# Optimization experiments

Measured on AMD Instinct MI355X. Metric: run time of the kernel, lower is better.

The kernel has to match this reference:

```python
import jax, jax.numpy as jnp
import numpy as np

PI = float(np.pi)

def erp_xyz_coords(h, w):
    # matches calculate_erp_coord: pixel grid -> uv -> unit-sphere xyz
    yy, xx = jnp.meshgrid(jnp.linspace(0.0, h - 1.0, h), jnp.linspace(0.0, w - 1.0, w), indexing='ij')
    u = (xx - (w / 2.0 + 0.5)) / w * 2.0 * PI
    v = (yy - (h / 2.0 + 0.5)) / h * PI
    xyz = jnp.stack([jnp.cos(v) * jnp.sin(u), jnp.sin(v), jnp.cos(v) * jnp.cos(u)], axis=-1)
    return xyz.reshape(h * w, 3)  # (HW, 3)


def setup_inputs() -> dict:
    key = jax.random.key(0)
    ks = jax.random.split(key, 16)
    B, C, H, W = 1, 128, 16, 32
    Nkv = 1280
    s = 0.02
    inp = {
        'erp_feature': jax.random.normal(ks[0], (B, C, H, W), jnp.float32),
        'ico_feature': jax.random.normal(ks[1], (B, Nkv, C), jnp.float32),
        'ico_coord': jax.random.normal(ks[2], (B, Nkv, 3), jnp.float32),
        # SA branch params (torch Linear: y = x @ W.T + b, W is (out,in))
        'Wq_sa': jax.random.normal(ks[3], (C, C), jnp.float32) * s,
        'Wkv_sa': jax.random.normal(ks[4], (2 * C, C), jnp.float32) * s,
        'proj_sa_w': jax.random.normal(ks[5], (C, C), jnp.float32) * s,
        'proj_sa_b': jnp.zeros((C,), jnp.float32),
        # DA branch params
        'Wq_da': jax.random.normal(ks[6], (C, C), jnp.float32) * s,
        'Wkv_da': jax.random.normal(ks[7], (2 * C, C), jnp.float32) * s,
        'Wdelta': jax.random.normal(ks[8], (C, 3), jnp.float32) * s,
        'proj_da_w': jax.random.normal(ks[9], (C, C), jnp.float32) * s,
        'proj_da_b': jnp.zeros((C,), jnp.float32),
        # gates
        'gate_sa_w': jax.random.normal(ks[10], (C, 2 * C), jnp.float32) * s,
        'gate_da_w': jax.random.normal(ks[11], (C, 2 * C), jnp.float32) * s,
    }
    return inp


def _forward(erp_feature, ico_feature, ico_coord,
             Wq_sa, Wkv_sa, proj_sa_w, proj_sa_b,
             Wq_da, Wkv_da, Wdelta, proj_da_w, proj_da_b,
             gate_sa_w, gate_da_w):
    B, C, H, W = erp_feature.shape
    Nq = H * W
    q = erp_feature.reshape(B, C, Nq).transpose(0, 2, 1)  # (B, Nq, C)
    qc = erp_xyz_coords(H, W)[None]                        # (1, Nq, 3) broadcasts over B

    # ---- SA branch (iteration = 1) ----
    q_sa = q @ Wq_sa.T                                     # (B, Nq, C)
    kv_sa = (ico_feature @ Wkv_sa.T).reshape(B, -1, 2, C)
    k_sa, v_sa = kv_sa[:, :, 0], kv_sa[:, :, 1]
    attn_sa = jax.nn.softmax(jnp.einsum('bqc,bkc->bqk', q_sa, k_sa) * (C ** -0.5), axis=-1)
    out_sa = jnp.einsum('bqk,bkc->bqc', attn_sa, v_sa)
    # faithful to torch: .transpose(1,2).reshape(B, Nq, C) scrambles layout
    out_sa = out_sa.transpose(0, 2, 1).reshape(B, Nq, C)
    sa = out_sa @ proj_sa_w.T + proj_sa_b

    # ---- DA branch (iteration = 1) ----
    q_da = q @ Wq_da.T
    kv_da = (ico_feature @ Wkv_da.T).reshape(B, -1, 2, C)
    k_da, v_da = kv_da[:, :, 0], kv_da[:, :, 1]
    # feature affinity: sum_c exp(-|q_c - k_c|)   -> (B, Nq, Nkv)
    feat_aff = jnp.exp(-jnp.abs(q_da[:, :, None, :] - k_da[:, None, :, :])).sum(-1)
    # positional term: (exp(-|dq - dk|) @ Wdelta.T).sum(-1) == exp(...) . Wdelta.sum(0)
    pos_exp = jnp.exp(-jnp.abs(qc[:, :, None, :] - ico_coord[:, None, :, :]))  # (B,Nq,Nkv,3)
    pos_aff = jnp.einsum('bqkt,t->bqk', pos_exp, Wdelta.sum(0))
    attn_da = jax.nn.softmax((feat_aff + pos_aff) * (1.0 / C), axis=-1)
    out_da = jnp.einsum('bqk,bkc->bqc', attn_da, v_da)
    da = out_da @ proj_da_w.T + proj_da_b

    # ---- gated fusion ----
    cat = jnp.concatenate([sa, da], axis=-1)               # (B, Nq, 2C)
    sa_factor = jax.nn.sigmoid(cat @ gate_sa_w.T)
    da_factor = jax.nn.sigmoid(cat @ gate_da_w.T)
    fused = sa_factor * sa + da_factor * da                # (B, Nq, C)
    return fused.reshape(B, H, W, C).transpose(0, 3, 1, 2)  # (B, C, H, W)


def reference(erp_feature, ico_feature, ico_coord,
              Wq_sa, Wkv_sa, proj_sa_w, proj_sa_b,
              Wq_da, Wkv_da, Wdelta, proj_da_w, proj_da_b,
              gate_sa_w, gate_da_w):
    return _forward(erp_feature, ico_feature, ico_coord,
                    Wq_sa, Wkv_sa, proj_sa_w, proj_sa_b,
                    Wq_da, Wkv_da, Wdelta, proj_da_w, proj_da_b,
                    gate_sa_w, gate_da_w)
```

## Files before the change

kernel.cpp:

```cpp
#include <hip/hip_runtime.h>
#include <math.h>

#define NQ   512
#define NKV  1280
#define CDIM 128

#define OFF_WDSUM 0
#define OFF_SUMS  16
#define OFF_QSA   1056
#define OFF_QDA   66592
#define OFF_KSAT  132128
#define OFF_VSA   295968
#define OFF_KDAT  459808
#define OFF_VDA   623648
#define OFF_OUT   787488

__global__ __launch_bounds__(256) void prep_kernel(
    const float* __restrict__ erp, const float* __restrict__ ico,
    const float* __restrict__ wq_sa, const float* __restrict__ wq_da,
    const float* __restrict__ wkv_sa, const float* __restrict__ wkv_da,
    const float* __restrict__ wdelta, float* __restrict__ ws)
{
  int bx = blockIdx.x, t = threadIdx.x;
  if (bx < 320) {
    __shared__ float x4[4 * CDIM];
    int k0 = bx * 4;
    for (int i = t; i < 512; i += 256) {
      int ky = i >> 7, j = i & 127;
      x4[j * 4 + ky] = ico[(k0 + ky) * CDIM + j];
    }
    __syncthreads();
    const float4* wsa4 = (const float4*)(wkv_sa + t * CDIM);
    const float4* wda4 = (const float4*)(wkv_da + t * CDIM);
    float as0=0,as1=0,as2=0,as3=0, ad0=0,ad1=0,ad2=0,ad3=0;
    #pragma unroll 4
    for (int j4 = 0; j4 < 32; ++j4) {
      float4 wsv = wsa4[j4];
      float4 wdv = wda4[j4];
      float4 x0 = *(const float4*)&x4[(j4 * 4 + 0) * 4];
      float4 x1 = *(const float4*)&x4[(j4 * 4 + 1) * 4];
      float4 x2 = *(const float4*)&x4[(j4 * 4 + 2) * 4];
      float4 x3 = *(const float4*)&x4[(j4 * 4 + 3) * 4];
      as0 = fmaf(wsv.x, x0.x, as0); as1 = fmaf(wsv.x, x0.y, as1);
      as2 = fmaf(wsv.x, x0.z, as2); as3 = fmaf(wsv.x, x0.w, as3);
      ad0 = fmaf(wdv.x, x0.x, ad0); ad1 = fmaf(wdv.x, x0.y, ad1);
      ad2 = fmaf(wdv.x, x0.z, ad2); ad3 = fmaf(wdv.x, x0.w, ad3);
      as0 = fmaf(wsv.y, x1.x, as0); as1 = fmaf(wsv.y, x1.y, as1);
      as2 = fmaf(wsv.y, x1.z, as2); as3 = fmaf(wsv.y, x1.w, as3);
      ad0 = fmaf(wdv.y, x1.x, ad0); ad1 = fmaf(wdv.y, x1.y, ad1);
      ad2 = fmaf(wdv.y, x1.z, ad2); ad3 = fmaf(wdv.y, x1.w, ad3);
      as0 = fmaf(wsv.z, x2.x, as0); as1 = fmaf(wsv.z, x2.y, as1);
      as2 = fmaf(wsv.z, x2.z, as2); as3 = fmaf(wsv.z, x2.w, as3);
      ad0 = fmaf(wdv.z, x2.x, ad0); ad1 = fmaf(wdv.z, x2.y, ad1);
      ad2 = fmaf(wdv.z, x2.z, ad2); ad3 = fmaf(wdv.z, x2.w, ad3);
      as0 = fmaf(wsv.w, x3.x, as0); as1 = fmaf(wsv.w, x3.y, as1);
      as2 = fmaf(wsv.w, x3.z, as2); as3 = fmaf(wsv.w, x3.w, as3);
      ad0 = fmaf(wdv.w, x3.x, ad0); ad1 = fmaf(wdv.w, x3.y, ad1);
      ad2 = fmaf(wdv.w, x3.z, ad2); ad3 = fmaf(wdv.w, x3.w, ad3);
    }
    if (t < 128) {
      *(float4*)(ws + OFF_KSAT + t * NKV + k0) = make_float4(as0, as1, as2, as3);
      *(float4*)(ws + OFF_KDAT + t * NKV + k0) = make_float4(ad0, ad1, ad2, ad3);
    } else {
      int c = t - 128;
      ws[OFF_VSA + (k0 + 0) * CDIM + c] = as0;
      ws[OFF_VSA + (k0 + 1) * CDIM + c] = as1;
      ws[OFF_VSA + (k0 + 2) * CDIM + c] = as2;
      ws[OFF_VSA + (k0 + 3) * CDIM + c] = as3;
      ws[OFF_VDA + (k0 + 0) * CDIM + c] = ad0;
      ws[OFF_VDA + (k0 + 1) * CDIM + c] = ad1;
      ws[OFF_VDA + (k0 + 2) * CDIM + c] = ad2;
      ws[OFF_VDA + (k0 + 3) * CDIM + c] = ad3;
    }
  } else if (bx < 448) {
    __shared__ float q4[4 * CDIM];
    int n0 = (bx - 320) * 4;
    for (int i = t; i < 512; i += 256)
      q4[i] = erp[(i >> 2) * NQ + n0 + (i & 3)];
    __syncthreads();
    const float* w = (t < 128) ? wq_sa : wq_da;
    int c = t & 127;
    const float4* w4 = (const float4*)(w + c * CDIM);
    float a0 = 0.f, a1 = 0.f, a2 = 0.f, a3 = 0.f;
    #pragma unroll 8
    for (int j4 = 0; j4 < 32; ++j4) {
      float4 wv = w4[j4];
      float4 q0 = *(const float4*)&q4[(j4 * 4 + 0) * 4];
      float4 q1 = *(const float4*)&q4[(j4 * 4 + 1) * 4];
      float4 q2 = *(const float4*)&q4[(j4 * 4 + 2) * 4];
      float4 q3 = *(const float4*)&q4[(j4 * 4 + 3) * 4];
      a0 = fmaf(wv.x, q0.x, a0); a1 = fmaf(wv.x, q0.y, a1);
      a2 = fmaf(wv.x, q0.z, a2); a3 = fmaf(wv.x, q0.w, a3);
      a0 = fmaf(wv.y, q1.x, a0); a1 = fmaf(wv.y, q1.y, a1);
      a2 = fmaf(wv.y, q1.z, a2); a3 = fmaf(wv.y, q1.w, a3);
      a0 = fmaf(wv.z, q2.x, a0); a1 = fmaf(wv.z, q2.y, a1);
      a2 = fmaf(wv.z, q2.z, a2); a3 = fmaf(wv.z, q2.w, a3);
      a0 = fmaf(wv.w, q3.x, a0); a1 = fmaf(wv.w, q3.y, a1);
      a2 = fmaf(wv.w, q3.z, a2); a3 = fmaf(wv.w, q3.w, a3);
    }
    float* o = ws + ((t < 128) ? OFF_QSA : OFF_QDA);
    o[(n0 + 0) * CDIM + c] = a0;
    o[(n0 + 1) * CDIM + c] = a1;
    o[(n0 + 2) * CDIM + c] = a2;
    o[(n0 + 3) * CDIM + c] = a3;
  } else if (bx == 448) {
    *(float4*)(ws + OFF_SUMS + t * 4) = make_float4(0.f, 0.f, 0.f, 0.f);
    if (t < 3) {
      float s = 0.f;
      for (int i = 0; i < 128; ++i) s += wdelta[i * 3 + t];
      ws[OFF_WDSUM + t] = s;
    }
  } else {
    int base = OFF_OUT + (bx - 449) * 1024 + t * 4;
    *(float4*)(ws + base) = make_float4(0.f, 0.f, 0.f, 0.f);
  }
}

__global__ __launch_bounds__(256) void attn_kernel(
    const float* __restrict__ coord, float* __restrict__ ws)
{
  __shared__ __align__(16) float qjf[4 * CDIM];
  __shared__ __align__(16) float psc[2][4][128];
  __shared__ __align__(16) float posk[4][128];
  __shared__ __align__(16) float se[4][128];
  __shared__ float red[2][4];
  __shared__ float qcr[4][3];
  __shared__ float wdl[3];
  int b = blockIdx.x, t = threadIdx.x;
  int br = (b < 1280) ? 1 : 0;
  int bb = br ? b : b - 1280;
  int g = bb / 10, z = bb - g * 10;
  int n0 = g * 4, k0 = z * 128;

  const float* qsrc = ws + (br ? OFF_QDA : OFF_QSA);
  for (int i = t; i < 512; i += 256) {
    int r = i & 3, j = i >> 2;
    qjf[j * 4 + r] = qsrc[(n0 + r) * CDIM + j];
  }
  if (br) {
    if (t < 4) {
      int n = n0 + t;
      float x = (float)(n & 31), y = (float)(n >> 5);
      float u  = (x - 16.5f) * 0.19634954084936207f;
      float vv = (y -  8.5f) * 0.19634954084936207f;
      float cv = cosf(vv);
      qcr[t][0] = cv * sinf(u);
      qcr[t][1] = sinf(vv);
      qcr[t][2] = cv * cosf(u);
    }
    if (t >= 64 && t < 67) wdl[t - 64] = ws[OFF_WDSUM + t - 64];
  }
  __syncthreads();

  int kl = t & 127, jh = t >> 7;
  int k = k0 + kl;
  {
    const float* kp = ws + (br ? OFF_KDAT : OFF_KSAT) + k + jh * 64 * NKV;
    const float4* qj = (const float4*)&qjf[jh * 64 * 4];
    float a0 = 0.f, a1 = 0.f, a2 = 0.f, a3 = 0.f;
    if (br) {
      #pragma unroll 4
      for (int j = 0; j < 64; ++j) {
        float kv = kp[j * NKV];
        float4 q = qj[j];
        a0 += __expf(-fabsf(q.x - kv)); a1 += __expf(-fabsf(q.y - kv));
        a2 += __expf(-fabsf(q.z - kv)); a3 += __expf(-fabsf(q.w - kv));
      }
    } else {
      #pragma unroll 8
      for (int j = 0; j < 64; ++j) {
        float kv = kp[j * NKV];
        float4 q = qj[j];
        a0 = fmaf(q.x, kv, a0); a1 = fmaf(q.y, kv, a1);
        a2 = fmaf(q.z, kv, a2); a3 = fmaf(q.w, kv, a3);
      }
    }
    psc[jh][0][kl] = a0; psc[jh][1][kl] = a1;
    psc[jh][2][kl] = a2; psc[jh][3][kl] = a3;
    if (br && jh == 1) {
      float c0 = coord[k * 3], c1 = coord[k * 3 + 1], c2 = coord[k * 3 + 2];
      float w0 = wdl[0], w1 = wdl[1], w2 = wdl[2];
      #pragma unroll
      for (int r = 0; r < 4; ++r)
        posk[r][kl] = w0 * __expf(-fabsf(qcr[r][0] - c0))
                    + w1 * __expf(-fabsf(qcr[r][1] - c1))
                    + w2 * __expf(-fabsf(qcr[r][2] - c2));
    }
  }
  __syncthreads();

  if (t < 128) {
    const float scl = 0.088388347648318447f;
    const float i128 = 0.0078125f;
    float s[4];
    #pragma unroll
    for (int r = 0; r < 4; ++r) {
      float tot = psc[0][r][t] + psc[1][r][t];
      float l = br ? (tot + posk[r][t]) * i128 : tot * scl;
      float e = __expf(l);
      se[r][t] = e;
      s[r] = e;
    }
    #pragma unroll
    for (int o = 32; o > 0; o >>= 1) {
      s[0] += __shfl_down(s[0], o, 64); s[1] += __shfl_down(s[1], o, 64);
      s[2] += __shfl_down(s[2], o, 64); s[3] += __shfl_down(s[3], o, 64);
    }
    if ((t & 63) == 0) {
      int w = t >> 6;
      red[w][0] = s[0]; red[w][1] = s[1]; red[w][2] = s[2]; red[w][3] = s[3];
    }
  }
  __syncthreads();
  if (t < 4)
    atomicAdd(ws + OFF_SUMS + br * 512 + n0 + t, red[0][t] + red[1][t]);

  int c = t & 127, h = t >> 7;
  const float* vp = ws + (br ? OFF_VDA : OFF_VSA) + k0 * CDIM + c;
  float acc0 = 0.f, acc1 = 0.f;
  #pragma unroll 4
  for (int ko = 0; ko < 128; ko += 4) {
    float4 pa = *(const float4*)&se[h][ko];
    float4 pb = *(const float4*)&se[h + 2][ko];
    float v0 = vp[(ko + 0) * CDIM];
    float v1 = vp[(ko + 1) * CDIM];
    float v2 = vp[(ko + 2) * CDIM];
    float v3 = vp[(ko + 3) * CDIM];
    acc0 = fmaf(pa.x, v0, acc0); acc1 = fmaf(pb.x, v0, acc1);
    acc0 = fmaf(pa.y, v1, acc0); acc1 = fmaf(pb.y, v1, acc1);
    acc0 = fmaf(pa.z, v2, acc0); acc1 = fmaf(pb.z, v2, acc1);
    acc0 = fmaf(pa.w, v3, acc0); acc1 = fmaf(pb.w, v3, acc1);
  }
  float* op = ws + OFF_OUT + br * (NQ * CDIM);
  atomicAdd(op + (n0 + h) * CDIM + c,     acc0);
  atomicAdd(op + (n0 + h + 2) * CDIM + c, acc1);
}

__global__ __launch_bounds__(256) void finalize_kernel(
    const float* __restrict__ psa, const float* __restrict__ bsa,
    const float* __restrict__ pda, const float* __restrict__ bda,
    const float* __restrict__ gsa, const float* __restrict__ gda,
    float* __restrict__ out, float* __restrict__ ws)
{
  __shared__ float sain[2][CDIM];
  __shared__ float dain[2][CDIM];
  __shared__ float cat[2][2 * CDIM];
  __shared__ float gl[2][2][CDIM];
  int i0 = blockIdx.x * 2, t = threadIdx.x;
  int h = t >> 7, c = t & 127;
  #pragma unroll
  for (int rr = 0; rr < 2; ++rr) {
    int i = i0 + rr;
    if (h == 0) {
      int row = (i & 3) * 128 + c;
      float s = ws[OFF_SUMS + row];
      sain[rr][c] = ws[OFF_OUT + row * CDIM + (i >> 2)] / s;
    } else {
      float s = ws[OFF_SUMS + 512 + i];
      dain[rr][c] = ws[OFF_OUT + NQ * CDIM + i * CDIM + c] / s;
    }
  }
  __syncthreads();
  {
    const float4* w4 = (const float4*)((h ? pda : psa) + c * CDIM);
    const float* in0 = h ? dain[0] : sain[0];
    const float* in1 = h ? dain[1] : sain[1];
    float a0 = 0, a1 = 0, b0 = 0, b1 = 0;
    #pragma unroll 8
    for (int j4 = 0; j4 < 32; ++j4) {
      float4 wv = w4[j4];
      float4 x0 = *(const float4*)&in0[j4 * 4];
      float4 x1 = *(const float4*)&in1[j4 * 4];
      a0 = fmaf(wv.x, x0.x, a0); a1 = fmaf(wv.y, x0.y, a1);
      a0 = fmaf(wv.z, x0.z, a0); a1 = fmaf(wv.w, x0.w, a1);
      b0 = fmaf(wv.x, x1.x, b0); b1 = fmaf(wv.y, x1.y, b1);
      b0 = fmaf(wv.z, x1.z, b0); b1 = fmaf(wv.w, x1.w, b1);
    }
    float bias = h ? bda[c] : bsa[c];
    cat[0][h * CDIM + c] = bias + a0 + a1;
    cat[1][h * CDIM + c] = bias + b0 + b1;
  }
  __syncthreads();
  {
    const float4* g4 = (const float4*)((h ? gda : gsa) + c * 2 * CDIM);
    float a0 = 0, a1 = 0, b0 = 0, b1 = 0;
    #pragma unroll 8
    for (int j4 = 0; j4 < 64; ++j4) {
      float4 gv = g4[j4];
      float4 c0 = *(const float4*)&cat[0][j4 * 4];
      float4 c1 = *(const float4*)&cat[1][j4 * 4];
      a0 = fmaf(gv.x, c0.x, a0); a1 = fmaf(gv.y, c0.y, a1);
      a0 = fmaf(gv.z, c0.z, a0); a1 = fmaf(gv.w, c0.w, a1);
      b0 = fmaf(gv.x, c1.x, b0); b1 = fmaf(gv.y, c1.y, b1);
      b0 = fmaf(gv.z, c1.z, b0); b1 = fmaf(gv.w, c1.w, b1);
    }
    gl[0][h][c] = 1.0f / (1.0f + __expf(-(a0 + a1)));
    gl[1][h][c] = 1.0f / (1.0f + __expf(-(b0 + b1)));
  }
  __syncthreads();
  {
    int i = i0 + h;
    out[c * NQ + i] = gl[h][0][c] * cat[h][c] + gl[h][1][c] * cat[h][CDIM + c];
  }
}

extern "C" void kernel_launch(void* const* d_in, const int* in_sizes, int n_in,
                              void* d_out, int out_size, void* d_ws, size_t ws_size,
                              hipStream_t stream)
{
  (void)in_sizes; (void)n_in; (void)out_size; (void)ws_size;
  const float* erp       = (const float*)d_in[0];
  const float* ico       = (const float*)d_in[1];
  const float* coord     = (const float*)d_in[2];
  const float* wq_sa     = (const float*)d_in[3];
  const float* wkv_sa    = (const float*)d_in[4];
  const float* proj_sa_w = (const float*)d_in[5];
  const float* proj_sa_b = (const float*)d_in[6];
  const float* wq_da     = (const float*)d_in[7];
  const float* wkv_da    = (const float*)d_in[8];
  const float* wdelta    = (const float*)d_in[9];
  const float* proj_da_w = (const float*)d_in[10];
  const float* proj_da_b = (const float*)d_in[11];
  const float* gate_sa   = (const float*)d_in[12];
  const float* gate_da   = (const float*)d_in[13];
  float* out = (float*)d_out;
  float* ws  = (float*)d_ws;

  hipLaunchKernelGGL(prep_kernel, dim3(577), dim3(256), 0, stream,
                     erp, ico, wq_sa, wq_da, wkv_sa, wkv_da, wdelta, ws);
  hipLaunchKernelGGL(attn_kernel, dim3(2560), dim3(256), 0, stream,
                     coord, ws);
  hipLaunchKernelGGL(finalize_kernel, dim3(256), dim3(256), 0, stream,
                     proj_sa_w, proj_sa_b, proj_da_w, proj_da_b,
                     gate_sa, gate_da, out, ws);
}
```

Before: 142.8 us.

## Retile attention to 8 queries x 256 keys per block with exp2 prescaling

Each attention block now handles 8 queries and 256 keys instead of 4 queries and 128 keys, with each thread owning a whole key across all 128 channels. This drops the split-channel partial-score smem stage and quarters the grid size. Each loaded K and V value is reused across twice as many queries, and there are fewer atomics per output. The DA branch and the softmax now use exp2f, with log2(e) folded into the stored Q/K projections and coordinates. The trade-offs are more registers per thread (8 accumulators), fewer blocks to spread across CUs, and interleaved SA/DA block ordering.

Measured after the change: 173.9 us. 21.7% more time.

```diff
diff --git a/kernel.cpp b/kernel.cpp
--- a/kernel.cpp
+++ b/kernel.cpp
@@ -4,6 +4,7 @@
 #define NQ   512
 #define NKV  1280
 #define CDIM 128
+#define L2E  1.4426950408889634f
 
 #define OFF_WDSUM 0
 #define OFF_SUMS  16
@@ -60,7 +61,8 @@
     }
     if (t < 128) {
       *(float4*)(ws + OFF_KSAT + t * NKV + k0) = make_float4(as0, as1, as2, as3);
-      *(float4*)(ws + OFF_KDAT + t * NKV + k0) = make_float4(ad0, ad1, ad2, ad3);
+      *(float4*)(ws + OFF_KDAT + t * NKV + k0) =
+          make_float4(ad0 * L2E, ad1 * L2E, ad2 * L2E, ad3 * L2E);
     } else {
       int c = t - 128;
       ws[OFF_VSA + (k0 + 0) * CDIM + c] = as0;
@@ -98,11 +100,12 @@
       a0 = fmaf(wv.w, q3.x, a0); a1 = fmaf(wv.w, q3.y, a1);
       a2 = fmaf(wv.w, q3.z, a2); a3 = fmaf(wv.w, q3.w, a3);
     }
+    float sc = (t < 128) ? 1.0f : L2E;
     float* o = ws + ((t < 128) ? OFF_QSA : OFF_QDA);
-    o[(n0 + 0) * CDIM + c] = a0;
-    o[(n0 + 1) * CDIM + c] = a1;
-    o[(n0 + 2) * CDIM + c] = a2;
-    o[(n0 + 3) * CDIM + c] = a3;
+    o[(n0 + 0) * CDIM + c] = a0 * sc;
+    o[(n0 + 1) * CDIM + c] = a1 * sc;
+    o[(n0 + 2) * CDIM + c] = a2 * sc;
+    o[(n0 + 3) * CDIM + c] = a3 * sc;
   } else if (bx == 448) {
     *(float4*)(ws + OFF_SUMS + t * 4) = make_float4(0.f, 0.f, 0.f, 0.f);
     if (t < 3) {
@@ -119,121 +122,159 @@
 __global__ __launch_bounds__(256) void attn_kernel(
     const float* __restrict__ coord, float* __restrict__ ws)
 {
-  __shared__ __align__(16) float qjf[4 * CDIM];
-  __shared__ __align__(16) float psc[2][4][128];
-  __shared__ __align__(16) float posk[4][128];
-  __shared__ __align__(16) float se[4][128];
-  __shared__ float red[2][4];
-  __shared__ float qcr[4][3];
+  __shared__ __align__(16) float qjf[128][8];
+  __shared__ __align__(16) float se[8][256];
+  __shared__ float red[4][8];
+  __shared__ float qcr[8][3];
   __shared__ float wdl[3];
   int b = blockIdx.x, t = threadIdx.x;
-  int br = (b < 1280) ? 1 : 0;
-  int bb = br ? b : b - 1280;
-  int g = bb / 10, z = bb - g * 10;
-  int n0 = g * 4, k0 = z * 128;
+  int br = b & 1;
+  int bb = b >> 1;
+  int g = bb / 5, z = bb - g * 5;
+  int n0 = g * 8, k0 = z * 256;
 
   const float* qsrc = ws + (br ? OFF_QDA : OFF_QSA);
-  for (int i = t; i < 512; i += 256) {
-    int r = i & 3, j = i >> 2;
-    qjf[j * 4 + r] = qsrc[(n0 + r) * CDIM + j];
+  {
+    int j = t & 127, r0 = t >> 7;
+    qjf[j][r0]     = qsrc[(n0 + r0)     * CDIM + j];
+    qjf[j][r0 + 2] = qsrc[(n0 + r0 + 2) * CDIM + j];
+    qjf[j][r0 + 4] = qsrc[(n0 + r0 + 4) * CDIM + j];
+    qjf[j][r0 + 6] = qsrc[(n0 + r0 + 6) * CDIM + j];
   }
   if (br) {
-    if (t < 4) {
+    if (t < 8) {
       int n = n0 + t;
       float x = (float)(n & 31), y = (float)(n >> 5);
       float u  = (x - 16.5f) * 0.19634954084936207f;
       float vv = (y -  8.5f) * 0.19634954084936207f;
       float cv = cosf(vv);
-      qcr[t][0] = cv * sinf(u);
-      qcr[t][1] = sinf(vv);
-      qcr[t][2] = cv * cosf(u);
-    }
-    if (t >= 64 && t < 67) wdl[t - 64] = ws[OFF_WDSUM + t - 64];
-  }
-  __syncthreads();
-
-  int kl = t & 127, jh = t >> 7;
-  int k = k0 + kl;
-  {
-    const float* kp = ws + (br ? OFF_KDAT : OFF_KSAT) + k + jh * 64 * NKV;
-    const float4* qj = (const float4*)&qjf[jh * 64 * 4];
-    float a0 = 0.f, a1 = 0.f, a2 = 0.f, a3 = 0.f;
-    if (br) {
-      #pragma unroll 4
-      for (int j = 0; j < 64; ++j) {
-        float kv = kp[j * NKV];
-        float4 q = qj[j];
-        a0 += __expf(-fabsf(q.x - kv)); a1 += __expf(-fabsf(q.y - kv));
-        a2 += __expf(-fabsf(q.z - kv)); a3 += __expf(-fabsf(q.w - kv));
-      }
-    } else {
-      #pragma unroll 8
-      for (int j = 0; j < 64; ++j) {
-        float kv = kp[j * NKV];
-        float4 q = qj[j];
-        a0 = fmaf(q.x, kv, a0); a1 = fmaf(q.y, kv, a1);
-        a2 = fmaf(q.z, kv, a2); a3 = fmaf(q.w, kv, a3);
-      }
-    }
-    psc[jh][0][kl] = a0; psc[jh][1][kl] = a1;
-    psc[jh][2][kl] = a2; psc[jh][3][kl] = a3;
-    if (br && jh == 1) {
-      float c0 = coord[k * 3], c1 = coord[k * 3 + 1], c2 = coord[k * 3 + 2];
-      float w0 = wdl[0], w1 = wdl[1], w2 = wdl[2];
-      #pragma unroll
-      for (int r = 0; r < 4; ++r)
-        posk[r][kl] = w0 * __expf(-fabsf(qcr[r][0] - c0))
-                    + w1 * __expf(-fabsf(qcr[r][1] - c1))
-                    + w2 * __expf(-fabsf(qcr[r][2] - c2));
-    }
-  }
-  __syncthreads();
-
-  if (t < 128) {
-    const float scl = 0.088388347648318447f;
-    const float i128 = 0.0078125f;
-    float s[4];
+      qcr[t][0] = cv * sinf(u) * L2E;
+      qcr[t][1] = sinf(vv) * L2E;
+      qcr[t][2] = cv * cosf(u) * L2E;
+    }
+    if (t >= 64 && t < 67) wdl[t - 64] = ws[OFF_WDSUM + (t - 64)];
+  }
+  __syncthreads();
+
+  int kl = t, k = k0 + kl;
+  float acc[8];
+  #pragma unroll
+  for (int r = 0; r < 8; ++r) acc[r] = 0.f;
+
+  if (br) {
+    const float* kp = ws + OFF_KDAT + k;
+    #pragma unroll 2
+    for (int j = 0; j < 128; ++j) {
+      float kv = kp[j * NKV];
+      float4 qa = *(const float4*)&qjf[j][0];
+      float4 qb = *(const float4*)&qjf[j][4];
+      acc[0] += exp2f(-fabsf(qa.x - kv));
+      acc[1] += exp2f(-fabsf(qa.y - kv));
+      acc[2] += exp2f(-fabsf(qa.z - kv));
+      acc[3] += exp2f(-fabsf(qa.w - kv));
+      acc[4] += exp2f(-fabsf(qb.x - kv));
+      acc[5] += exp2f(-fabsf(qb.y - kv));
+      acc[6] += exp2f(-fabsf(qb.z - kv));
+      acc[7] += exp2f(-fabsf(qb.w - kv));
+    }
+  } else {
+    const float* kp = ws + OFF_KSAT + k;
+    #pragma unroll 4
+    for (int j = 0; j < 128; ++j) {
+      float kv = kp[j * NKV];
+      float4 qa = *(const float4*)&qjf[j][0];
+      float4 qb = *(const float4*)&qjf[j][4];
+      acc[0] = fmaf(qa.x, kv, acc[0]);
+      acc[1] = fmaf(qa.y, kv, acc[1]);
+      acc[2] = fmaf(qa.z, kv, acc[2]);
+      acc[3] = fmaf(qa.w, kv, acc[3]);
+      acc[4] = fmaf(qb.x, kv, acc[4]);
+      acc[5] = fmaf(qb.y, kv, acc[5]);
+      acc[6] = fmaf(qb.z, kv, acc[6]);
+      acc[7] = fmaf(qb.w, kv, acc[7]);
+    }
+  }
+
+  float e[8];
+  if (br) {
+    float c0 = coord[3 * k]     * L2E;
+    float c1 = coord[3 * k + 1] * L2E;
+    float c2 = coord[3 * k + 2] * L2E;
+    float w0 = wdl[0], w1 = wdl[1], w2 = wdl[2];
     #pragma unroll
-    for (int r = 0; r < 4; ++r) {
-      float tot = psc[0][r][t] + psc[1][r][t];
-      float l = br ? (tot + posk[r][t]) * i128 : tot * scl;
-      float e = __expf(l);
-      se[r][t] = e;
-      s[r] = e;
-    }
+    for (int r = 0; r < 8; ++r) {
+      float pos = w0 * exp2f(-fabsf(qcr[r][0] - c0))
+                + w1 * exp2f(-fabsf(qcr[r][1] - c1))
+                + w2 * exp2f(-fabsf(qcr[r][2] - c2));
+      e[r] = exp2f((acc[r] + pos) * (L2E / 128.0f));
+    }
+  } else {
+    const float scl = 0.088388347648318447f * L2E;
     #pragma unroll
-    for (int o = 32; o > 0; o >>= 1) {
-      s[0] += __shfl_down(s[0], o, 64); s[1] += __shfl_down(s[1], o, 64);
-      s[2] += __shfl_down(s[2], o, 64); s[3] += __shfl_down(s[3], o, 64);
-    }
-    if ((t & 63) == 0) {
-      int w = t >> 6;
-      red[w][0] = s[0]; red[w][1] = s[1]; red[w][2] = s[2]; red[w][3] = s[3];
-    }
-  }
-  __syncthreads();
-  if (t < 4)
-    atomicAdd(ws + OFF_SUMS + br * 512 + n0 + t, red[0][t] + red[1][t]);
+    for (int r = 0; r < 8; ++r) e[r] = exp2f(acc[r] * scl);
+  }
+  #pragma unroll
+  for (int r = 0; r < 8; ++r) se[r][kl] = e[r];
+
+  float s[8];
+  #pragma unroll
+  for (int r = 0; r < 8; ++r) s[r] = e[r];
+  #pragma unroll
+  for (int o = 32; o > 0; o >>= 1) {
+    #pragma unroll
+    for (int r = 0; r < 8; ++r) s[r] += __shfl_down(s[r], o, 64);
+  }
+  if ((t & 63) == 0) {
+    int w = t >> 6;
+    #pragma unroll
+    for (int r = 0; r < 8; ++r) red[w][r] = s[r];
+  }
+  __syncthreads();
+  if (t < 8)
+    atomicAdd(ws + OFF_SUMS + br * 512 + n0 + t,
+              red[0][t] + red[1][t] + red[2][t] + red[3][t]);
 
   int c = t & 127, h = t >> 7;
-  const float* vp = ws + (br ? OFF_VDA : OFF_VSA) + k0 * CDIM + c;
-  float acc0 = 0.f, acc1 = 0.f;
-  #pragma unroll 4
+  int kb = h * 128;
+  const float* vp = ws + (br ? OFF_VDA : OFF_VSA) + (k0 + kb) * CDIM + c;
+  float a[8];
+  #pragma unroll
+  for (int r = 0; r < 8; ++r) a[r] = 0.f;
+  #pragma unroll 2
   for (int ko = 0; ko < 128; ko += 4) {
-    float4 pa = *(const float4*)&se[h][ko];
-    float4 pb = *(const float4*)&se[h + 2][ko];
+    float4 p0 = *(const float4*)&se[0][kb + ko];
+    float4 p1 = *(const float4*)&se[1][kb + ko];
+    float4 p2 = *(const float4*)&se[2][kb + ko];
+    float4 p3 = *(const float4*)&se[3][kb + ko];
+    float4 p4 = *(const float4*)&se[4][kb + ko];
+    float4 p5 = *(const float4*)&se[5][kb + ko];
+    float4 p6 = *(const float4*)&se[6][kb + ko];
+    float4 p7 = *(const float4*)&se[7][kb + ko];
     float v0 = vp[(ko + 0) * CDIM];
     float v1 = vp[(ko + 1) * CDIM];
     float v2 = vp[(ko + 2) * CDIM];
     float v3 = vp[(ko + 3) * CDIM];
-    acc0 = fmaf(pa.x, v0, acc0); acc1 = fmaf(pb.x, v0, acc1);
-    acc0 = fmaf(pa.y, v1, acc0); acc1 = fmaf(pb.y, v1, acc1);
-    acc0 = fmaf(pa.z, v2, acc0); acc1 = fmaf(pb.z, v2, acc1);
-    acc0 = fmaf(pa.w, v3, acc0); acc1 = fmaf(pb.w, v3, acc1);
-  }
-  float* op = ws + OFF_OUT + br * (NQ * CDIM);
-  atomicAdd(op + (n0 + h) * CDIM + c,     acc0);
-  atomicAdd(op + (n0 + h + 2) * CDIM + c, acc1);
+    a[0] = fmaf(p0.x, v0, a[0]); a[0] = fmaf(p0.y, v1, a[0]);
+    a[0] = fmaf(p0.z, v2, a[0]); a[0] = fmaf(p0.w, v3, a[0]);
+    a[1] = fmaf(p1.x, v0, a[1]); a[1] = fmaf(p1.y, v1, a[1]);
+    a[1] = fmaf(p1.z, v2, a[1]); a[1] = fmaf(p1.w, v3, a[1]);
+    a[2] = fmaf(p2.x, v0, a[2]); a[2] = fmaf(p2.y, v1, a[2]);
+    a[2] = fmaf(p2.z, v2, a[2]); a[2] = fmaf(p2.w, v3, a[2]);
+    a[3] = fmaf(p3.x, v0, a[3]); a[3] = fmaf(p3.y, v1, a[3]);
+    a[3] = fmaf(p3.z, v2, a[3]); a[3] = fmaf(p3.w, v3, a[3]);
+    a[4] = fmaf(p4.x, v0, a[4]); a[4] = fmaf(p4.y, v1, a[4]);
+    a[4] = fmaf(p4.z, v2, a[4]); a[4] = fmaf(p4.w, v3, a[4]);
+    a[5] = fmaf(p5.x, v0, a[5]); a[5] = fmaf(p5.y, v1, a[5]);
+    a[5] = fmaf(p5.z, v2, a[5]); a[5] = fmaf(p5.w, v3, a[5]);
+    a[6] = fmaf(p6.x, v0, a[6]); a[6] = fmaf(p6.y, v1, a[6]);
+    a[6] = fmaf(p6.z, v2, a[6]); a[6] = fmaf(p6.w, v3, a[6]);
+    a[7] = fmaf(p7.x, v0, a[7]); a[7] = fmaf(p7.y, v1, a[7]);
+    a[7] = fmaf(p7.z, v2, a[7]); a[7] = fmaf(p7.w, v3, a[7]);
+  }
+  float* op = ws + OFF_OUT + br * (NQ * CDIM) + c;
+  #pragma unroll
+  for (int r = 0; r < 8; ++r)
+    atomicAdd(op + (n0 + r) * CDIM, a[r]);
 }
 
 __global__ __launch_bounds__(256) void finalize_kernel(
@@ -328,7 +369,7 @@
 
   hipLaunchKernelGGL(prep_kernel, dim3(577), dim3(256), 0, stream,
                      erp, ico, wq_sa, wq_da, wkv_sa, wkv_da, wdelta, ws);
-  hipLaunchKernelGGL(attn_kernel, dim3(2560), dim3(256), 0, stream,
+  hipLaunchKernelGGL(attn_kernel, dim3(640), dim3(256), 0, stream,
                      coord, ws);
   hipLaunchKernelGGL(finalize_kernel, dim3(256), dim3(256), 0, stream,
                      proj_sa_w, proj_sa_b, proj_da_w, proj_da_b,
```

## Restructure attention: row-major K, transposed V, 256-key tiles, exp2 with prescaling

Applied to the files above, without the earlier changes.

K matrices are now stored row-major and V transposed, so each attention thread reads its key row as contiguous float4 vectors and the PV stage reads V columns as float4. Each block now covers 256 keys with one key per thread over the full channel depth, instead of splitting channels across two halves. That removes the psc/posk shared-memory passes and one barrier, and halves the number of blocks. DA queries, keys and coordinates are prescaled by log2(e) so exp2f replaces __expf. The trade-offs are uncoalesced strided reads of K across threads and more work per block.

New measurement: 171.4 us. +20.0%, slower.

```diff
diff --git a/kernel.cpp b/kernel.cpp
--- a/kernel.cpp
+++ b/kernel.cpp
@@ -4,15 +4,16 @@
 #define NQ   512
 #define NKV  1280
 #define CDIM 128
+#define L2E  1.4426950408889634f
 
 #define OFF_WDSUM 0
 #define OFF_SUMS  16
 #define OFF_QSA   1056
 #define OFF_QDA   66592
-#define OFF_KSAT  132128
-#define OFF_VSA   295968
-#define OFF_KDAT  459808
-#define OFF_VDA   623648
+#define OFF_KSA   132128
+#define OFF_VSAT  295968
+#define OFF_KDA   459808
+#define OFF_VDAT  623648
 #define OFF_OUT   787488
 
 __global__ __launch_bounds__(256) void prep_kernel(
@@ -59,18 +60,19 @@
       ad2 = fmaf(wdv.w, x3.z, ad2); ad3 = fmaf(wdv.w, x3.w, ad3);
     }
     if (t < 128) {
-      *(float4*)(ws + OFF_KSAT + t * NKV + k0) = make_float4(as0, as1, as2, as3);
-      *(float4*)(ws + OFF_KDAT + t * NKV + k0) = make_float4(ad0, ad1, ad2, ad3);
+      int c = t;
+      ws[OFF_KSA + (k0 + 0) * CDIM + c] = as0;
+      ws[OFF_KSA + (k0 + 1) * CDIM + c] = as1;
+      ws[OFF_KSA + (k0 + 2) * CDIM + c] = as2;
+      ws[OFF_KSA + (k0 + 3) * CDIM + c] = as3;
+      ws[OFF_KDA + (k0 + 0) * CDIM + c] = ad0 * L2E;
+      ws[OFF_KDA + (k0 + 1) * CDIM + c] = ad1 * L2E;
+      ws[OFF_KDA + (k0 + 2) * CDIM + c] = ad2 * L2E;
+      ws[OFF_KDA + (k0 + 3) * CDIM + c] = ad3 * L2E;
     } else {
       int c = t - 128;
-      ws[OFF_VSA + (k0 + 0) * CDIM + c] = as0;
-      ws[OFF_VSA + (k0 + 1) * CDIM + c] = as1;
-      ws[OFF_VSA + (k0 + 2) * CDIM + c] = as2;
-      ws[OFF_VSA + (k0 + 3) * CDIM + c] = as3;
-      ws[OFF_VDA + (k0 + 0) * CDIM + c] = ad0;
-      ws[OFF_VDA + (k0 + 1) * CDIM + c] = ad1;
-      ws[OFF_VDA + (k0 + 2) * CDIM + c] = ad2;
-      ws[OFF_VDA + (k0 + 3) * CDIM + c] = ad3;
+      *(float4*)(ws + OFF_VSAT + c * NKV + k0) = make_float4(as0, as1, as2, as3);
+      *(float4*)(ws + OFF_VDAT + c * NKV + k0) = make_float4(ad0, ad1, ad2, ad3);
     }
   } else if (bx < 448) {
     __shared__ float q4[4 * CDIM];
@@ -98,11 +100,12 @@
       a0 = fmaf(wv.w, q3.x, a0); a1 = fmaf(wv.w, q3.y, a1);
       a2 = fmaf(wv.w, q3.z, a2); a3 = fmaf(wv.w, q3.w, a3);
     }
+    float sc = (t < 128) ? 1.0f : L2E;
     float* o = ws + ((t < 128) ? OFF_QSA : OFF_QDA);
-    o[(n0 + 0) * CDIM + c] = a0;
-    o[(n0 + 1) * CDIM + c] = a1;
-    o[(n0 + 2) * CDIM + c] = a2;
-    o[(n0 + 3) * CDIM + c] = a3;
+    o[(n0 + 0) * CDIM + c] = a0 * sc;
+    o[(n0 + 1) * CDIM + c] = a1 * sc;
+    o[(n0 + 2) * CDIM + c] = a2 * sc;
+    o[(n0 + 3) * CDIM + c] = a3 * sc;
   } else if (bx == 448) {
     *(float4*)(ws + OFF_SUMS + t * 4) = make_float4(0.f, 0.f, 0.f, 0.f);
     if (t < 3) {
@@ -119,23 +122,22 @@
 __global__ __launch_bounds__(256) void attn_kernel(
     const float* __restrict__ coord, float* __restrict__ ws)
 {
-  __shared__ __align__(16) float qjf[4 * CDIM];
-  __shared__ __align__(16) float psc[2][4][128];
-  __shared__ __align__(16) float posk[4][128];
-  __shared__ __align__(16) float se[4][128];
-  __shared__ float red[2][4];
+  __shared__ __align__(16) float qjf[128][4];
+  __shared__ __align__(16) float se[4][256];
+  __shared__ float red[4][4];
   __shared__ float qcr[4][3];
   __shared__ float wdl[3];
   int b = blockIdx.x, t = threadIdx.x;
-  int br = (b < 1280) ? 1 : 0;
-  int bb = br ? b : b - 1280;
-  int g = bb / 10, z = bb - g * 10;
-  int n0 = g * 4, k0 = z * 128;
+  int br = b & 1;
+  int bb = b >> 1;
+  int g = bb / 5, z = bb - g * 5;
+  int n0 = g * 4, k0 = z * 256;
 
   const float* qsrc = ws + (br ? OFF_QDA : OFF_QSA);
-  for (int i = t; i < 512; i += 256) {
-    int r = i & 3, j = i >> 2;
-    qjf[j * 4 + r] = qsrc[(n0 + r) * CDIM + j];
+  {
+    int j = t & 127, rh = t >> 7;
+    qjf[j][rh]     = qsrc[(n0 + rh)     * CDIM + j];
+    qjf[j][rh + 2] = qsrc[(n0 + rh + 2) * CDIM + j];
   }
   if (br) {
     if (t < 4) {
@@ -144,96 +146,128 @@
       float u  = (x - 16.5f) * 0.19634954084936207f;
       float vv = (y -  8.5f) * 0.19634954084936207f;
       float cv = cosf(vv);
-      qcr[t][0] = cv * sinf(u);
-      qcr[t][1] = sinf(vv);
-      qcr[t][2] = cv * cosf(u);
-    }
-    if (t >= 64 && t < 67) wdl[t - 64] = ws[OFF_WDSUM + t - 64];
-  }
-  __syncthreads();
-
-  int kl = t & 127, jh = t >> 7;
-  int k = k0 + kl;
-  {
-    const float* kp = ws + (br ? OFF_KDAT : OFF_KSAT) + k + jh * 64 * NKV;
-    const float4* qj = (const float4*)&qjf[jh * 64 * 4];
-    float a0 = 0.f, a1 = 0.f, a2 = 0.f, a3 = 0.f;
-    if (br) {
-      #pragma unroll 4
-      for (int j = 0; j < 64; ++j) {
-        float kv = kp[j * NKV];
-        float4 q = qj[j];
-        a0 += __expf(-fabsf(q.x - kv)); a1 += __expf(-fabsf(q.y - kv));
-        a2 += __expf(-fabsf(q.z - kv)); a3 += __expf(-fabsf(q.w - kv));
-      }
-    } else {
-      #pragma unroll 8
-      for (int j = 0; j < 64; ++j) {
-        float kv = kp[j * NKV];
-        float4 q = qj[j];
-        a0 = fmaf(q.x, kv, a0); a1 = fmaf(q.y, kv, a1);
-        a2 = fmaf(q.z, kv, a2); a3 = fmaf(q.w, kv, a3);
-      }
-    }
-    psc[jh][0][kl] = a0; psc[jh][1][kl] = a1;
-    psc[jh][2][kl] = a2; psc[jh][3][kl] = a3;
-    if (br && jh == 1) {
-      float c0 = coord[k * 3], c1 = coord[k * 3 + 1], c2 = coord[k * 3 + 2];
-      float w0 = wdl[0], w1 = wdl[1], w2 = wdl[2];
-      #pragma unroll
-      for (int r = 0; r < 4; ++r)
-        posk[r][kl] = w0 * __expf(-fabsf(qcr[r][0] - c0))
-                    + w1 * __expf(-fabsf(qcr[r][1] - c1))
-                    + w2 * __expf(-fabsf(qcr[r][2] - c2));
-    }
-  }
-  __syncthreads();
-
-  if (t < 128) {
-    const float scl = 0.088388347648318447f;
-    const float i128 = 0.0078125f;
-    float s[4];
-    #pragma unroll
-    for (int r = 0; r < 4; ++r) {
-      float tot = psc[0][r][t] + psc[1][r][t];
-      float l = br ? (tot + posk[r][t]) * i128 : tot * scl;
-      float e = __expf(l);
-      se[r][t] = e;
-      s[r] = e;
-    }
-    #pragma unroll
-    for (int o = 32; o > 0; o >>= 1) {
-      s[0] += __shfl_down(s[0], o, 64); s[1] += __shfl_down(s[1], o, 64);
-      s[2] += __shfl_down(s[2], o, 64); s[3] += __shfl_down(s[3], o, 64);
-    }
-    if ((t & 63) == 0) {
-      int w = t >> 6;
-      red[w][0] = s[0]; red[w][1] = s[1]; red[w][2] = s[2]; red[w][3] = s[3];
-    }
+      qcr[t][0] = cv * sinf(u) * L2E;
+      qcr[t][1] = sinf(vv) * L2E;
+      qcr[t][2] = cv * cosf(u) * L2E;
+    }
+    if (t >= 64 && t < 67) wdl[t - 64] = ws[OFF_WDSUM + (t - 64)];
+  }
+  __syncthreads();
+
+  int k = k0 + t;
+  float acc0 = 0.f, acc1 = 0.f, acc2 = 0.f, acc3 = 0.f;
+
+  if (br) {
+    const float4* kp = (const float4*)(ws + OFF_KDA + k * CDIM);
+    #pragma unroll 4
+    for (int j4 = 0; j4 < 32; ++j4) {
+      float4 kv = kp[j4];
+      float4 q0 = *(const float4*)qjf[j4 * 4 + 0];
+      float4 q1 = *(const float4*)qjf[j4 * 4 + 1];
+      float4 q2 = *(const float4*)qjf[j4 * 4 + 2];
+      float4 q3 = *(const float4*)qjf[j4 * 4 + 3];
+      acc0 += exp2f(-fabsf(q0.x - kv.x)); acc0 += exp2f(-fabsf(q1.x - kv.y));
+      acc0 += exp2f(-fabsf(q2.x - kv.z)); acc0 += exp2f(-fabsf(q3.x - kv.w));
+      acc1 += exp2f(-fabsf(q0.y - kv.x)); acc1 += exp2f(-fabsf(q1.y - kv.y));
+      acc1 += exp2f(-fabsf(q2.y - kv.z)); acc1 += exp2f(-fabsf(q3.y - kv.w));
+      acc2 += exp2f(-fabsf(q0.z - kv.x)); acc2 += exp2f(-fabsf(q1.z - kv.y));
+      acc2 += exp2f(-fabsf(q2.z - kv.z)); acc2 += exp2f(-fabsf(q3.z - kv.w));
+      acc3 += exp2f(-fabsf(q0.w - kv.x)); acc3 += exp2f(-fabsf(q1.w - kv.y));
+      acc3 += exp2f(-fabsf(q2.w - kv.z)); acc3 += exp2f(-fabsf(q3.w - kv.w));
+    }
+  } else {
+    const float4* kp = (const float4*)(ws + OFF_KSA + k * CDIM);
+    #pragma unroll 4
+    for (int j4 = 0; j4 < 32; ++j4) {
+      float4 kv = kp[j4];
+      float4 q0 = *(const float4*)qjf[j4 * 4 + 0];
+      float4 q1 = *(const float4*)qjf[j4 * 4 + 1];
+      float4 q2 = *(const float4*)qjf[j4 * 4 + 2];
+      float4 q3 = *(const float4*)qjf[j4 * 4 + 3];
+      acc0 = fmaf(q0.x, kv.x, acc0); acc0 = fmaf(q1.x, kv.y, acc0);
+      acc0 = fmaf(q2.x, kv.z, acc0); acc0 = fmaf(q3.x, kv.w, acc0);
+      acc1 = fmaf(q0.y, kv.x, acc1); acc1 = fmaf(q1.y, kv.y, acc1);
+      acc1 = fmaf(q2.y, kv.z, acc1); acc1 = fmaf(q3.y, kv.w, acc1);
+      acc2 = fmaf(q0.z, kv.x, acc2); acc2 = fmaf(q1.z, kv.y, acc2);
+      acc2 = fmaf(q2.z, kv.z, acc2); acc2 = fmaf(q3.z, kv.w, acc2);
+      acc3 = fmaf(q0.w, kv.x, acc3); acc3 = fmaf(q1.w, kv.y, acc3);
+      acc3 = fmaf(q2.w, kv.z, acc3); acc3 = fmaf(q3.w, kv.w, acc3);
+    }
+  }
+
+  float e0, e1, e2, e3;
+  if (br) {
+    float c0 = coord[3 * k]     * L2E;
+    float c1 = coord[3 * k + 1] * L2E;
+    float c2 = coord[3 * k + 2] * L2E;
+    float w0 = wdl[0], w1 = wdl[1], w2 = wdl[2];
+    float p0 = w0 * exp2f(-fabsf(qcr[0][0] - c0))
+             + w1 * exp2f(-fabsf(qcr[0][1] - c1))
+             + w2 * exp2f(-fabsf(qcr[0][2] - c2));
+    float p1 = w0 * exp2f(-fabsf(qcr[1][0] - c0))
+             + w1 * exp2f(-fabsf(qcr[1][1] - c1))
+             + w2 * exp2f(-fabsf(qcr[1][2] - c2));
+    float p2 = w0 * exp2f(-fabsf(qcr[2][0] - c0))
+             + w1 * exp2f(-fabsf(qcr[2][1] - c1))
+             + w2 * exp2f(-fabsf(qcr[2][2] - c2));
+    float p3 = w0 * exp2f(-fabsf(qcr[3][0] - c0))
+             + w1 * exp2f(-fabsf(qcr[3][1] - c1))
+             + w2 * exp2f(-fabsf(qcr[3][2] - c2));
+    const float lsc = L2E / 128.0f;
+    e0 = exp2f((acc0 + p0) * lsc);
+    e1 = exp2f((acc1 + p1) * lsc);
+    e2 = exp2f((acc2 + p2) * lsc);
+    e3 = exp2f((acc3 + p3) * lsc);
+  } else {
+    const float scl = 0.088388347648318447f * L2E;
+    e0 = exp2f(acc0 * scl);
+    e1 = exp2f(acc1 * scl);
+    e2 = exp2f(acc2 * scl);
+    e3 = exp2f(acc3 * scl);
+  }
+  se[0][t] = e0; se[1][t] = e1; se[2][t] = e2; se[3][t] = e3;
+
+  float s0 = e0, s1 = e1, s2 = e2, s3 = e3;
+  #pragma unroll
+  for (int o = 32; o > 0; o >>= 1) {
+    s0 += __shfl_down(s0, o, 64); s1 += __shfl_down(s1, o, 64);
+    s2 += __shfl_down(s2, o, 64); s3 += __shfl_down(s3, o, 64);
+  }
+  if ((t & 63) == 0) {
+    int w = t >> 6;
+    red[w][0] = s0; red[w][1] = s1; red[w][2] = s2; red[w][3] = s3;
   }
   __syncthreads();
   if (t < 4)
-    atomicAdd(ws + OFF_SUMS + br * 512 + n0 + t, red[0][t] + red[1][t]);
+    atomicAdd(ws + OFF_SUMS + br * 512 + n0 + t,
+              red[0][t] + red[1][t] + red[2][t] + red[3][t]);
 
   int c = t & 127, h = t >> 7;
-  const float* vp = ws + (br ? OFF_VDA : OFF_VSA) + k0 * CDIM + c;
-  float acc0 = 0.f, acc1 = 0.f;
+  int kb = h * 128;
+  const float4* vp = (const float4*)(ws + (br ? OFF_VDAT : OFF_VSAT)
+                                     + c * NKV + k0 + kb);
+  float a0 = 0.f, a1 = 0.f, a2 = 0.f, a3 = 0.f;
   #pragma unroll 4
-  for (int ko = 0; ko < 128; ko += 4) {
-    float4 pa = *(const float4*)&se[h][ko];
-    float4 pb = *(const float4*)&se[h + 2][ko];
-    float v0 = vp[(ko + 0) * CDIM];
-    float v1 = vp[(ko + 1) * CDIM];
-    float v2 = vp[(ko + 2) * CDIM];
-    float v3 = vp[(ko + 3) * CDIM];
-    acc0 = fmaf(pa.x, v0, acc0); acc1 = fmaf(pb.x, v0, acc1);
-    acc0 = fmaf(pa.y, v1, acc0); acc1 = fmaf(pb.y, v1, acc1);
-    acc0 = fmaf(pa.z, v2, acc0); acc1 = fmaf(pb.z, v2, acc1);
-    acc0 = fmaf(pa.w, v3, acc0); acc1 = fmaf(pb.w, v3, acc1);
-  }
-  float* op = ws + OFF_OUT + br * (NQ * CDIM);
-  atomicAdd(op + (n0 + h) * CDIM + c,     acc0);
-  atomicAdd(op + (n0 + h + 2) * CDIM + c, acc1);
+  for (int q4 = 0; q4 < 32; ++q4) {
+    float4 vv = vp[q4];
+    float4 p0 = *(const float4*)&se[0][kb + q4 * 4];
+    float4 p1 = *(const float4*)&se[1][kb + q4 * 4];
+    float4 p2 = *(const float4*)&se[2][kb + q4 * 4];
+    float4 p3 = *(const float4*)&se[3][kb + q4 * 4];
+    a0 = fmaf(p0.x, vv.x, a0); a0 = fmaf(p0.y, vv.y, a0);
+    a0 = fmaf(p0.z, vv.z, a0); a0 = fmaf(p0.w, vv.w, a0);
+    a1 = fmaf(p1.x, vv.x, a1); a1 = fmaf(p1.y, vv.y, a1);
+    a1 = fmaf(p1.z, vv.z, a1); a1 = fmaf(p1.w, vv.w, a1);
+    a2 = fmaf(p2.x, vv.x, a2); a2 = fmaf(p2.y, vv.y, a2);
+    a2 = fmaf(p2.z, vv.z, a2); a2 = fmaf(p2.w, vv.w, a2);
+    a3 = fmaf(p3.x, vv.x, a3); a3 = fmaf(p3.y, vv.y, a3);
+    a3 = fmaf(p3.z, vv.z, a3); a3 = fmaf(p3.w, vv.w, a3);
+  }
+  float* op = ws + OFF_OUT + br * (NQ * CDIM) + c;
+  atomicAdd(op + (n0 + 0) * CDIM, a0);
+  atomicAdd(op + (n0 + 1) * CDIM, a1);
+  atomicAdd(op + (n0 + 2) * CDIM, a2);
+  atomicAdd(op + (n0 + 3) * CDIM, a3);
 }
 
 __global__ __launch_bounds__(256) void finalize_kernel(
@@ -328,7 +362,7 @@
 
   hipLaunchKernelGGL(prep_kernel, dim3(577), dim3(256), 0, stream,
                      erp, ico, wq_sa, wq_da, wkv_sa, wkv_da, wdelta, ws);
-  hipLaunchKernelGGL(attn_kernel, dim3(2560), dim3(256), 0, stream,
+  hipLaunchKernelGGL(attn_kernel, dim3(1280), dim3(256), 0, stream,
                      coord, ws);
   hipLaunchKernelGGL(finalize_kernel, dim3(256), dim3(256), 0, stream,
                      proj_sa_w, proj_sa_b, proj_da_w, proj_da_b,
```

## Widen attention key tiles to 256 and interleave SA/DA blocks

Applied to the files above, without the earlier changes.

Each attention block now covers 256 keys instead of 128, and each thread computes the full 128-dim dot/abs-exp sum for its own key, so the split-j partial-score buffer and its extra reduction are gone. The grid is halved to 1280 blocks and SA/DA blocks are interleaved by blockIdx parity to balance the heavier DA work across the machine. The PV stage now has each thread accumulate all 4 query rows over a 128-key half. This halves the number of atomic writes per output element, but each thread does a longer serial loop and there are fewer blocks to hide latency.

After: 147.0 us. +2.9%, slower.

```diff
diff --git a/kernel.cpp b/kernel.cpp
--- a/kernel.cpp
+++ b/kernel.cpp
@@ -119,23 +119,22 @@
 __global__ __launch_bounds__(256) void attn_kernel(
     const float* __restrict__ coord, float* __restrict__ ws)
 {
-  __shared__ __align__(16) float qjf[4 * CDIM];
-  __shared__ __align__(16) float psc[2][4][128];
-  __shared__ __align__(16) float posk[4][128];
-  __shared__ __align__(16) float se[4][128];
-  __shared__ float red[2][4];
+  __shared__ __align__(16) float qjf[128][4];
+  __shared__ __align__(16) float se[4][256];
+  __shared__ float red[4][4];
   __shared__ float qcr[4][3];
   __shared__ float wdl[3];
   int b = blockIdx.x, t = threadIdx.x;
-  int br = (b < 1280) ? 1 : 0;
-  int bb = br ? b : b - 1280;
-  int g = bb / 10, z = bb - g * 10;
-  int n0 = g * 4, k0 = z * 128;
+  int br = b & 1;
+  int bb = b >> 1;
+  int g = bb / 5, z = bb - g * 5;
+  int n0 = g * 4, k0 = z * 256;
 
   const float* qsrc = ws + (br ? OFF_QDA : OFF_QSA);
-  for (int i = t; i < 512; i += 256) {
-    int r = i & 3, j = i >> 2;
-    qjf[j * 4 + r] = qsrc[(n0 + r) * CDIM + j];
+  {
+    int j = t & 127, rh = t >> 7;
+    qjf[j][rh]     = qsrc[(n0 + rh)     * CDIM + j];
+    qjf[j][rh + 2] = qsrc[(n0 + rh + 2) * CDIM + j];
   }
   if (br) {
     if (t < 4) {
@@ -148,92 +147,110 @@
       qcr[t][1] = sinf(vv);
       qcr[t][2] = cv * cosf(u);
     }
-    if (t >= 64 && t < 67) wdl[t - 64] = ws[OFF_WDSUM + t - 64];
-  }
-  __syncthreads();
-
-  int kl = t & 127, jh = t >> 7;
-  int k = k0 + kl;
-  {
-    const float* kp = ws + (br ? OFF_KDAT : OFF_KSAT) + k + jh * 64 * NKV;
-    const float4* qj = (const float4*)&qjf[jh * 64 * 4];
-    float a0 = 0.f, a1 = 0.f, a2 = 0.f, a3 = 0.f;
-    if (br) {
-      #pragma unroll 4
-      for (int j = 0; j < 64; ++j) {
-        float kv = kp[j * NKV];
-        float4 q = qj[j];
-        a0 += __expf(-fabsf(q.x - kv)); a1 += __expf(-fabsf(q.y - kv));
-        a2 += __expf(-fabsf(q.z - kv)); a3 += __expf(-fabsf(q.w - kv));
-      }
-    } else {
-      #pragma unroll 8
-      for (int j = 0; j < 64; ++j) {
-        float kv = kp[j * NKV];
-        float4 q = qj[j];
-        a0 = fmaf(q.x, kv, a0); a1 = fmaf(q.y, kv, a1);
-        a2 = fmaf(q.z, kv, a2); a3 = fmaf(q.w, kv, a3);
-      }
-    }
-    psc[jh][0][kl] = a0; psc[jh][1][kl] = a1;
-    psc[jh][2][kl] = a2; psc[jh][3][kl] = a3;
-    if (br && jh == 1) {
-      float c0 = coord[k * 3], c1 = coord[k * 3 + 1], c2 = coord[k * 3 + 2];
-      float w0 = wdl[0], w1 = wdl[1], w2 = wdl[2];
-      #pragma unroll
-      for (int r = 0; r < 4; ++r)
-        posk[r][kl] = w0 * __expf(-fabsf(qcr[r][0] - c0))
-                    + w1 * __expf(-fabsf(qcr[r][1] - c1))
-                    + w2 * __expf(-fabsf(qcr[r][2] - c2));
-    }
-  }
-  __syncthreads();
-
-  if (t < 128) {
+    if (t >= 64 && t < 67) wdl[t - 64] = ws[OFF_WDSUM + (t - 64)];
+  }
+  __syncthreads();
+
+  int k = k0 + t;
+  float acc0 = 0.f, acc1 = 0.f, acc2 = 0.f, acc3 = 0.f;
+
+  if (br) {
+    const float* kt = ws + OFF_KDAT + k;
+    #pragma unroll 4
+    for (int j = 0; j < 128; ++j) {
+      float kv = kt[j * NKV];
+      float4 q = *(const float4*)qjf[j];
+      acc0 += __expf(-fabsf(q.x - kv));
+      acc1 += __expf(-fabsf(q.y - kv));
+      acc2 += __expf(-fabsf(q.z - kv));
+      acc3 += __expf(-fabsf(q.w - kv));
+    }
+  } else {
+    const float* kt = ws + OFF_KSAT + k;
+    #pragma unroll 8
+    for (int j = 0; j < 128; ++j) {
+      float kv = kt[j * NKV];
+      float4 q = *(const float4*)qjf[j];
+      acc0 = fmaf(q.x, kv, acc0);
+      acc1 = fmaf(q.y, kv, acc1);
+      acc2 = fmaf(q.z, kv, acc2);
+      acc3 = fmaf(q.w, kv, acc3);
+    }
+  }
+
+  float e0, e1, e2, e3;
+  if (br) {
+    float c0 = coord[3 * k], c1 = coord[3 * k + 1], c2 = coord[3 * k + 2];
+    float w0 = wdl[0], w1 = wdl[1], w2 = wdl[2];
+    float p0 = w0 * __expf(-fabsf(qcr[0][0] - c0))
+             + w1 * __expf(-fabsf(qcr[0][1] - c1))
+             + w2 * __expf(-fabsf(qcr[0][2] - c2));
+    float p1 = w0 * __expf(-fabsf(qcr[1][0] - c0))
+             + w1 * __expf(-fabsf(qcr[1][1] - c1))
+             + w2 * __expf(-fabsf(qcr[1][2] - c2));
+    float p2 = w0 * __expf(-fabsf(qcr[2][0] - c0))
+             + w1 * __expf(-fabsf(qcr[2][1] - c1))
+             + w2 * __expf(-fabsf(qcr[2][2] - c2));
+    float p3 = w0 * __expf(-fabsf(qcr[3][0] - c0))
+             + w1 * __expf(-fabsf(qcr[3][1] - c1))
+             + w2 * __expf(-fabsf(qcr[3][2] - c2));
+    const float i128 = 0.0078125f;
+    e0 = __expf((acc0 + p0) * i128);
+    e1 = __expf((acc1 + p1) * i128);
+    e2 = __expf((acc2 + p2) * i128);
+    e3 = __expf((acc3 + p3) * i128);
+  } else {
     const float scl = 0.088388347648318447f;
-    const float i128 = 0.0078125f;
-    float s[4];
-    #pragma unroll
-    for (int r = 0; r < 4; ++r) {
-      float tot = psc[0][r][t] + psc[1][r][t];
-      float l = br ? (tot + posk[r][t]) * i128 : tot * scl;
-      float e = __expf(l);
-      se[r][t] = e;
-      s[r] = e;
-    }
-    #pragma unroll
-    for (int o = 32; o > 0; o >>= 1) {
-      s[0] += __shfl_down(s[0], o, 64); s[1] += __shfl_down(s[1], o, 64);
-      s[2] += __shfl_down(s[2], o, 64); s[3] += __shfl_down(s[3], o, 64);
-    }
-    if ((t & 63) == 0) {
-      int w = t >> 6;
-      red[w][0] = s[0]; red[w][1] = s[1]; red[w][2] = s[2]; red[w][3] = s[3];
-    }
+    e0 = __expf(acc0 * scl);
+    e1 = __expf(acc1 * scl);
+    e2 = __expf(acc2 * scl);
+    e3 = __expf(acc3 * scl);
+  }
+  se[0][t] = e0; se[1][t] = e1; se[2][t] = e2; se[3][t] = e3;
+
+  float s0 = e0, s1 = e1, s2 = e2, s3 = e3;
+  #pragma unroll
+  for (int o = 32; o > 0; o >>= 1) {
+    s0 += __shfl_down(s0, o, 64); s1 += __shfl_down(s1, o, 64);
+    s2 += __shfl_down(s2, o, 64); s3 += __shfl_down(s3, o, 64);
+  }
+  if ((t & 63) == 0) {
+    int w = t >> 6;
+    red[w][0] = s0; red[w][1] = s1; red[w][2] = s2; red[w][3] = s3;
   }
   __syncthreads();
   if (t < 4)
-    atomicAdd(ws + OFF_SUMS + br * 512 + n0 + t, red[0][t] + red[1][t]);
+    atomicAdd(ws + OFF_SUMS + br * 512 + n0 + t,
+              red[0][t] + red[1][t] + red[2][t] + red[3][t]);
 
   int c = t & 127, h = t >> 7;
-  const float* vp = ws + (br ? OFF_VDA : OFF_VSA) + k0 * CDIM + c;
-  float acc0 = 0.f, acc1 = 0.f;
-  #pragma unroll 4
+  int kb = h * 128;
+  const float* vp = ws + (br ? OFF_VDA : OFF_VSA) + (k0 + kb) * CDIM + c;
+  float a0 = 0.f, a1 = 0.f, a2 = 0.f, a3 = 0.f;
+  #pragma unroll 2
   for (int ko = 0; ko < 128; ko += 4) {
-    float4 pa = *(const float4*)&se[h][ko];
-    float4 pb = *(const float4*)&se[h + 2][ko];
+    float4 p0 = *(const float4*)&se[0][kb + ko];
+    float4 p1 = *(const float4*)&se[1][kb + ko];
+    float4 p2 = *(const float4*)&se[2][kb + ko];
+    float4 p3 = *(const float4*)&se[3][kb + ko];
     float v0 = vp[(ko + 0) * CDIM];
     float v1 = vp[(ko + 1) * CDIM];
     float v2 = vp[(ko + 2) * CDIM];
     float v3 = vp[(ko + 3) * CDIM];
-    acc0 = fmaf(pa.x, v0, acc0); acc1 = fmaf(pb.x, v0, acc1);
-    acc0 = fmaf(pa.y, v1, acc0); acc1 = fmaf(pb.y, v1, acc1);
-    acc0 = fmaf(pa.z, v2, acc0); acc1 = fmaf(pb.z, v2, acc1);
-    acc0 = fmaf(pa.w, v3, acc0); acc1 = fmaf(pb.w, v3, acc1);
-  }
-  float* op = ws + OFF_OUT + br * (NQ * CDIM);
-  atomicAdd(op + (n0 + h) * CDIM + c,     acc0);
-  atomicAdd(op + (n0 + h + 2) * CDIM + c, acc1);
+    a0 = fmaf(p0.x, v0, a0); a0 = fmaf(p0.y, v1, a0);
+    a0 = fmaf(p0.z, v2, a0); a0 = fmaf(p0.w, v3, a0);
+    a1 = fmaf(p1.x, v0, a1); a1 = fmaf(p1.y, v1, a1);
+    a1 = fmaf(p1.z, v2, a1); a1 = fmaf(p1.w, v3, a1);
+    a2 = fmaf(p2.x, v0, a2); a2 = fmaf(p2.y, v1, a2);
+    a2 = fmaf(p2.z, v2, a2); a2 = fmaf(p2.w, v3, a2);
+    a3 = fmaf(p3.x, v0, a3); a3 = fmaf(p3.y, v1, a3);
+    a3 = fmaf(p3.z, v2, a3); a3 = fmaf(p3.w, v3, a3);
+  }
+  float* op = ws + OFF_OUT + br * (NQ * CDIM) + c;
+  atomicAdd(op + (n0 + 0) * CDIM, a0);
+  atomicAdd(op + (n0 + 1) * CDIM, a1);
+  atomicAdd(op + (n0 + 2) * CDIM, a2);
+  atomicAdd(op + (n0 + 3) * CDIM, a3);
 }
 
 __global__ __launch_bounds__(256) void finalize_kernel(
@@ -328,7 +345,7 @@
 
   hipLaunchKernelGGL(prep_kernel, dim3(577), dim3(256), 0, stream,
                      erp, ico, wq_sa, wq_da, wkv_sa, wkv_da, wdelta, ws);
-  hipLaunchKernelGGL(attn_kernel, dim3(2560), dim3(256), 0, stream,
+  hipLaunchKernelGGL(attn_kernel, dim3(1280), dim3(256), 0, stream,
                      coord, ws);
   hipLaunchKernelGGL(finalize_kernel, dim3(256), dim3(256), 0, stream,
                      proj_sa_w, proj_sa_b, proj_da_w, proj_da_b,
```
